# Kernel tuning notes

Hardware: AMD Instinct MI355X
Metric: run time of the kernel (lower is better)

Reference implementation:

```python
import jax, jax.numpy as jnp
import numpy as np

DN = ('NHWC', 'HWIO', 'NHWC')
EPS = 1e-3  # Keras BatchNormalization default epsilon


def conv2d(x, w):
    return jax.lax.conv_general_dilated(x, w, (1, 1), 'SAME', dimension_numbers=DN)


def hard_sigmoid(x):
    # Keras ConvLSTM2D default recurrent_activation
    return jnp.clip(0.2 * x + 0.5, 0.0, 1.0)


def convlstm2d(x, Wx, Wh, b):
    """Keras ConvLSTM2D, return_sequences=True. x: (B,T,H,W,C).
    Wx: (3,3,C,4F) input kernel, Wh: (3,3,F,4F) recurrent kernel, b: (4F,).
    Gate order (Keras): i, f, c, o."""
    B, T, H, W, C = x.shape
    F = Wh.shape[2]
    # input-to-gate convs for all timesteps in one batched conv
    xg = conv2d(x.reshape(B * T, H, W, C), Wx) + b          # (B*T,H,W,4F)
    xg = xg.reshape(B, T, H, W, 4 * F).transpose(1, 0, 2, 3, 4)  # (T,B,H,W,4F)

    def step(carry, xg_t):
        h, c = carry
        g = xg_t + conv2d(h, Wh)                            # (B,H,W,4F)
        i, f, cc, o = jnp.split(g, 4, axis=-1)
        i = hard_sigmoid(i)
        f = hard_sigmoid(f)
        o = hard_sigmoid(o)
        c = f * c + i * jnp.tanh(cc)
        h = o * jnp.tanh(c)
        return (h, c), h

    h0 = jnp.zeros((B, H, W, F), x.dtype)
    (_, _), hs = jax.lax.scan(step, (h0, h0), xg)           # hs: (T,B,H,W,F)
    return hs.transpose(1, 0, 2, 3, 4)


def batchnorm(x, gamma, beta):
    # training-mode BN over all axes except channel (last)
    mu = x.mean(axis=(0, 1, 2, 3), keepdims=True)
    var = x.var(axis=(0, 1, 2, 3), keepdims=True)
    return gamma * (x - mu) * jax.lax.rsqrt(var + EPS) + beta


def setup_inputs() -> dict:
    key = jax.random.key(0)
    B, T, H, W, C = 4, 8, 16, 16, 256
    F = 256
    ks = jax.random.split(key, 10)
    s = 0.02
    inp = {
        'input_tensor': jax.random.normal(ks[0], (B, T, H, W, C), jnp.float32),
        'Wx1': jax.random.normal(ks[1], (3, 3, C, 4 * F), jnp.float32) * s,
        'Wh1': jax.random.normal(ks[2], (3, 3, F, 4 * F), jnp.float32) * s,
        'b1': jnp.zeros((4 * F,), jnp.float32),
        'g1': jnp.ones((F,), jnp.float32),
        'be1': jnp.zeros((F,), jnp.float32),
        'Wx2': jax.random.normal(ks[3], (3, 3, F, 4 * F), jnp.float32) * s,
        'Wh2': jax.random.normal(ks[4], (3, 3, F, 4 * F), jnp.float32) * s,
        'b2': jnp.zeros((4 * F,), jnp.float32),
        'g2': jnp.ones((F,), jnp.float32),
        'be2': jnp.zeros((F,), jnp.float32),
        'Wx3': jax.random.normal(ks[5], (3, 3, F, 4 * F), jnp.float32) * s,
        'Wh3': jax.random.normal(ks[6], (3, 3, F, 4 * F), jnp.float32) * s,
        'b3': jnp.zeros((4 * F,), jnp.float32),
        'g3': jnp.ones((F,), jnp.float32),
        'be3': jnp.zeros((F,), jnp.float32),
    }
    return inp


def reference(input_tensor, Wx1, Wh1, b1, g1, be1,
              Wx2, Wh2, b2, g2, be2,
              Wx3, Wh3, b3, g3, be3):
    x = batchnorm(convlstm2d(input_tensor, Wx1, Wh1, b1), g1, be1)
    x = batchnorm(convlstm2d(x, Wx2, Wh2, b2), g2, be2)
    x = batchnorm(convlstm2d(x, Wx3, Wh3, b3), g3, be3)
    return x
```

## Files before the change

### kernel.cpp

```cpp
#include <hip/hip_runtime.h>

#define HW      256
#define COUT    1024
#define TSTEPS  8
#define BN_EPS  1e-3f
#define KTOT    2304

typedef unsigned short u16;
typedef unsigned int   u32;
typedef __attribute__((ext_vector_type(8))) _Float16 v8h;
typedef __attribute__((ext_vector_type(4))) float v4f;

__device__ __forceinline__ u16 f2h(float x) {
    _Float16 h = (_Float16)x; return *(u16*)&h;
}
__device__ __forceinline__ float h2f(u16 u) {
    _Float16 h = *(_Float16*)&u; return (float)h;
}
__device__ __forceinline__ float hsig(float x) {
    return fminf(fmaxf(0.2f * x + 0.5f, 0.f), 1.f);
}

typedef __attribute__((address_space(1))) const unsigned int gas_u32;
typedef __attribute__((address_space(3))) unsigned int las_u32;
__device__ __forceinline__ void gl16(const void* g, void* l) {
    __builtin_amdgcn_global_load_lds((gas_u32*)g, (las_u32*)l, 16, 0, 0);
}

__global__ __launch_bounds__(256, 2) void conv_big_k(
    const u16* __restrict__ apad,
    const u16* __restrict__ wT,
    const float* __restrict__ bias,
    u16* __restrict__ out)
{
    constexpr int KQ = 36;
    __shared__ u16 lds[2 * 16384];

    const int bid = blockIdx.x;
    const int xcd = bid & 7, idx = bid >> 3;
    const int by = (xcd >> 1) * 2 + (idx & 1);
    const int bx = (xcd & 1) * 32 + (idx >> 1);
    const int m0 = bx * 128, n0 = by * 128;
    const int tid = threadIdx.x, lane = tid & 63, w = tid >> 6;
    const int wr = w >> 1, wc = w & 1;
    const int lr = lane >> 3;
    const int g  = (lane & 7) ^ lr;
    const int fr = lane & 15, kc = lane >> 4;

    const char* a_src[4];
    #pragma unroll
    for (int i = 0; i < 4; ++i) {
        int m = m0 + w * 32 + i * 8 + lr;
        int img = m >> 8, pix = m & 255, yy = pix >> 4, xx = pix & 15;
        a_src[i] = (const char*)apad + ((((long)img * 18 + yy) * 18 + xx) * 256 + g * 8) * 2;
    }
    const char* b_src[4];
    #pragma unroll
    for (int i = 0; i < 4; ++i) {
        int n = n0 + w * 32 + i * 8 + lr;
        b_src[i] = (const char*)wT + ((long)n * KTOT + g * 8) * 2;
    }

    int aro[4][2], bro[4][2];
    #pragma unroll
    for (int mi = 0; mi < 4; ++mi) {
        int rl = wr * 64 + mi * 16 + fr;
        #pragma unroll
        for (int ks = 0; ks < 2; ++ks)
            aro[mi][ks] = rl * 128 + ((((ks << 2) | kc) ^ (fr & 7)) << 4);
    }
    #pragma unroll
    for (int ni = 0; ni < 4; ++ni) {
        int nr = wc * 64 + ni * 16 + fr;
        #pragma unroll
        for (int ks = 0; ks < 2; ++ks)
            bro[ni][ks] = 16384 + nr * 128 + ((((ks << 2) | kc) ^ (fr & 7)) << 4);
    }

    v4f acc[4][4];
    #pragma unroll
    for (int mi = 0; mi < 4; ++mi)
        #pragma unroll
        for (int ni = 0; ni < 4; ++ni) acc[mi][ni] = (v4f)0.f;

#define STAGE_B(J) { int j_ = (J); int dxy = j_ >> 2, c64 = j_ & 3;           \
    int dy = (dxy * 11) >> 5; int dx = dxy - dy * 3;                          \
    int aoff = ((dy * 18 + dx) * 256 + c64 * 64) * 2; int boff = j_ * 128;    \
    char* base = (char*)lds + (j_ & 1) * 32768;                               \
    _Pragma("unroll") for (int i = 0; i < 4; ++i)                             \
        gl16(a_src[i] + aoff, base + (w * 32 + i * 8) * 128);                 \
    _Pragma("unroll") for (int i = 0; i < 4; ++i)                             \
        gl16(b_src[i] + boff, base + 16384 + (w * 32 + i * 8) * 128); }

#define COMPUTE_B(J) { const char* base = (const char*)lds + ((J) & 1) * 32768; \
    v8h af[4][2], bf[4][2];                                                   \
    _Pragma("unroll") for (int mi = 0; mi < 4; ++mi)                          \
        _Pragma("unroll") for (int ks = 0; ks < 2; ++ks)                      \
            af[mi][ks] = *(const v8h*)(base + aro[mi][ks]);                   \
    _Pragma("unroll") for (int ni = 0; ni < 4; ++ni)                          \
        _Pragma("unroll") for (int ks = 0; ks < 2; ++ks)                      \
            bf[ni][ks] = *(const v8h*)(base + bro[ni][ks]);                   \
    __builtin_amdgcn_s_setprio(1);                                            \
    _Pragma("unroll") for (int ks = 0; ks < 2; ++ks)                          \
    _Pragma("unroll") for (int mi = 0; mi < 4; ++mi)                          \
    _Pragma("unroll") for (int ni = 0; ni < 4; ++ni)                          \
        acc[mi][ni] = __builtin_amdgcn_mfma_f32_16x16x32_f16(af[mi][ks], bf[ni][ks], acc[mi][ni], 0, 0, 0); \
    __builtin_amdgcn_s_setprio(0); }

    STAGE_B(0);
    for (int kq = 0; kq < KQ - 1; ++kq) {
        asm volatile("s_waitcnt vmcnt(0)" ::: "memory");
        __builtin_amdgcn_s_barrier();
        __builtin_amdgcn_sched_barrier(0);
        STAGE_B(kq + 1);
        COMPUTE_B(kq);
    }
    asm volatile("s_waitcnt vmcnt(0)" ::: "memory");
    __builtin_amdgcn_s_barrier();
    __builtin_amdgcn_sched_barrier(0);
    COMPUTE_B(KQ - 1);
#undef STAGE_B
#undef COMPUTE_B

    #pragma unroll
    for (int mi = 0; mi < 4; ++mi) {
        #pragma unroll
        for (int ni = 0; ni < 4; ++ni) {
            int mrow = m0 + wr * 64 + mi * 16 + ((lane >> 4) << 2);
            int ncol = n0 + wc * 64 + ni * 16 + fr;
            float b0 = bias[(ncol & 3) * 256 + (ncol >> 2)];
            #pragma unroll
            for (int r = 0; r < 4; ++r)
                out[(long)(mrow + r) * COUT + ncol] = f2h(acc[mi][ni][r] + b0);
        }
    }
}

__global__ __launch_bounds__(512) void rec_fused_k(
    const u16* __restrict__ ph_in,
    const u16* __restrict__ wTf,
    const u16* __restrict__ xg,
    float* __restrict__ cbuf,
    u16* __restrict__ hs16,
    u16* __restrict__ ph_out,
    int t)
{
    __shared__ u16 lds[6 * 4096];

    const int bid = blockIdx.x;
    const int by = (bid & 7) * 2 + ((bid >> 3) & 1);
    const int bx = bid >> 4;
    const int m0 = bx * 64, n0 = by * 64;
    const int tid = threadIdx.x, lane = tid & 63, w = tid >> 6;
    const int wr = w >> 2, wc = w & 3;
    const int fr = lane & 15, kc = lane >> 4;

    const int f4  = n0 + wc * 16 + (lane & 12);
    const int fch = f4 >> 2;
    int erow[2]; long xrow[2], cidx[2];
    uint2 xb_pre[2];
    float c_pre[2];
    #pragma unroll
    for (int mi = 0; mi < 2; ++mi) {
        erow[mi] = m0 + wr * 32 + mi * 16 + ((lane >> 4) << 2) + (lane & 3);
        int img = erow[mi] >> 8, pix = erow[mi] & 255;
        xrow[mi] = ((long)(img * TSTEPS + t) * HW + pix);
        cidx[mi] = (long)erow[mi] * 256 + fch;
        xb_pre[mi] = *(const uint2*)&xg[xrow[mi] * COUT + f4];
        c_pre[mi]  = cbuf[cidx[mi]];
    }

    const char* a_src;
    {
        int rt = tid >> 3;
        int gg = (tid & 7) ^ (rt & 7);
        int m = m0 + rt;
        int img = m >> 8, pix = m & 255, yy = pix >> 4, xx = pix & 15;
        a_src = (const char*)ph_in + ((((long)img * 18 + yy) * 18 + xx) * 256 + gg * 8) * 2;
    }
    const char* b_base = (const char*)wTf + ((long)(by * 4 + wc) * 72) * 1024 + lane * 16;

    int aro[2][2];
    #pragma unroll
    for (int mi = 0; mi < 2; ++mi)
        #pragma unroll
        for (int ks = 0; ks < 2; ++ks)
            aro[mi][ks] = (wr * 32 + mi * 16 + fr) * 128 + ((((ks << 2) | kc) ^ (fr & 7)) << 4);

    v4f acc0 = (v4f)0.f, acc1 = (v4f)0.f;

#define STAGE_A(J, BUF) { int j_ = (J); int dxy = j_ >> 2, c64 = j_ & 3;      \
    int dy = (dxy * 11) >> 5; int dx = dxy - dy * 3;                          \
    int aoff = ((dy * 18 + dx) * 256 + c64 * 64) * 2;                         \
    gl16(a_src + aoff, (char*)lds + (BUF) * 8192 + w * 1024); }

#define LDB(J, R0, R1) { R0 = *(const v8h*)(b_base + (2 * (J)) * 1024);       \
                         R1 = *(const v8h*)(b_base + (2 * (J) + 1) * 1024); }

#define CKQ(BUF, C0, C1) {                                                    \
    const char* base_ = (const char*)lds + (BUF) * 8192;                      \
    v8h af00_ = *(const v8h*)(base_ + aro[0][0]);                             \
    v8h af10_ = *(const v8h*)(base_ + aro[1][0]);                             \
    v8h af01_ = *(const v8h*)(base_ + aro[0][1]);                             \
    v8h af11_ = *(const v8h*)(base_ + aro[1][1]);                             \
    __builtin_amdgcn_s_setprio(1);                                            \
    acc0 = __builtin_amdgcn_mfma_f32_16x16x32_f16(af00_, C0, acc0, 0, 0, 0);  \
    acc1 = __builtin_amdgcn_mfma_f32_16x16x32_f16(af10_, C0, acc1, 0, 0, 0);  \
    acc0 = __builtin_amdgcn_mfma_f32_16x16x32_f16(af01_, C1, acc0, 0, 0, 0);  \
    acc1 = __builtin_amdgcn_mfma_f32_16x16x32_f16(af11_, C1, acc1, 0, 0, 0);  \
    __builtin_amdgcn_s_setprio(0); }

#define BODY2(J2, BC, BS, Ca0, Ca1, Cb0, Cb1, La0, La1, Lb0, Lb1) {           \
    int q0_ = 2 * (J2);                                                       \
    asm volatile("s_waitcnt vmcnt(6)" ::: "memory");                          \
    __builtin_amdgcn_s_barrier();                                             \
    __builtin_amdgcn_sched_barrier(0);                                        \
    LDB(q0_ + 4, La0, La1); LDB(q0_ + 5, Lb0, Lb1);                           \
    STAGE_A(q0_ + 4, BS); STAGE_A(q0_ + 5, (BS) + 1);                         \
    CKQ(BC,       Ca0, Ca1);                                                  \
    CKQ((BC) + 1, Cb0, Cb1); }

    v8h S00, S01, S02, S03, S10, S11, S12, S13, S20, S21, S22, S23;
    LDB(0, S00, S01); LDB(1, S02, S03); STAGE_A(0, 0); STAGE_A(1, 1);
    LDB(2, S10, S11); LDB(3, S12, S13); STAGE_A(2, 2); STAGE_A(3, 3);

    for (int j = 0; j < 5; ++j) {
        BODY2(3 * j,     0, 4, S00, S01, S02, S03, S20, S21, S22, S23);
        BODY2(3 * j + 1, 2, 0, S10, S11, S12, S13, S00, S01, S02, S03);
        BODY2(3 * j + 2, 4, 2, S20, S21, S22, S23, S10, S11, S12, S13);
    }
    BODY2(15, 0, 4, S00, S01, S02, S03, S20, S21, S22, S23);
    asm volatile("s_waitcnt vmcnt(6)" ::: "memory");
    __builtin_amdgcn_s_barrier();
    __builtin_amdgcn_sched_barrier(0);
    CKQ(2, S10, S11);
    CKQ(3, S12, S13);
    asm volatile("s_waitcnt vmcnt(0)" ::: "memory");
    __builtin_amdgcn_s_barrier();
    __builtin_amdgcn_sched_barrier(0);
    CKQ(4, S20, S21);
    CKQ(5, S22, S23);
#undef STAGE_A
#undef LDB
#undef CKQ
#undef BODY2

    v4f accA[2] = {acc0, acc1};
    const bool gl0 = lane & 1, gl1 = lane & 2;
    #pragma unroll
    for (int mi = 0; mi < 2; ++mi) {
        float V0 = accA[mi][0], V1 = accA[mi][1];
        float V2 = accA[mi][2], V3 = accA[mi][3];
        float x0 = __shfl_xor(V0, 1), x1 = __shfl_xor(V1, 1);
        float x2 = __shfl_xor(V2, 1), x3 = __shfl_xor(V3, 1);
        float a0 = gl0 ? x1 : V0;
        float a1 = gl0 ? V1 : x0;
        float a2 = gl0 ? x3 : V2;
        float a3 = gl0 ? V3 : x2;
        float s0 = __shfl_xor(a0, 2), s1 = __shfl_xor(a1, 2);
        float s2 = __shfl_xor(a2, 2), s3 = __shfl_xor(a3, 2);
        float Ti = gl1 ? s2 : a0;
        float Tf = gl1 ? s3 : a1;
        float Tc = gl1 ? a2 : s0;
        float To = gl1 ? a3 : s1;

        float pi = Ti + h2f((u16)(xb_pre[mi].x & 0xffff));
        float pf = Tf + h2f((u16)(xb_pre[mi].x >> 16));
        float pc = Tc + h2f((u16)(xb_pre[mi].y & 0xffff));
        float po = To + h2f((u16)(xb_pre[mi].y >> 16));
        float c = hsig(pf) * c_pre[mi] + hsig(pi) * tanhf(pc);
        float h = hsig(po) * tanhf(c);
        cbuf[cidx[mi]] = c;
        u16 hv = f2h(h);
        hs16[xrow[mi] * 256 + fch] = hv;
        int pix = erow[mi] & 255, img = erow[mi] >> 8;
        ph_out[(((long)img * 18 + (pix >> 4) + 1) * 18 + (pix & 15) + 1) * 256 + fch] = hv;
    }
}

__global__ __launch_bounds__(256) void gates0_k(
    const u16* __restrict__ xg, float* __restrict__ cbuf,
    u16* __restrict__ hs16, u16* __restrict__ ph_out)
{
    int idx = blockIdx.x * 256 + threadIdx.x;
    int fch = idx & 255, row = idx >> 8;
    int img = row >> 8, pix = row & 255;
    long xrow = (long)(img * TSTEPS) * HW + pix;
    uint2 xb = *(const uint2*)&xg[xrow * COUT + fch * 4];
    float pi = h2f((u16)(xb.x & 0xffff));
    float pc = h2f((u16)(xb.y & 0xffff));
    float po = h2f((u16)(xb.y >> 16));
    float c = hsig(pi) * tanhf(pc);
    float h = hsig(po) * tanhf(c);
    cbuf[(long)row * 256 + fch] = c;
    u16 hv = f2h(h);
    hs16[xrow * 256 + fch] = hv;
    int yy = pix >> 4, xx = pix & 15;
    ph_out[(((long)img * 18 + yy + 1) * 18 + xx + 1) * 256 + fch] = hv;
}

__global__ __launch_bounds__(256) void wprep_all_k(
    const float* __restrict__ wx, const float* __restrict__ wh,
    u16* __restrict__ wT, u16* __restrict__ wTf)
{
    int kq = blockIdx.x;
    int by = blockIdx.y;
    if (by < 4) {
        int k0 = kq * 32;
        int np = by * 256 + threadIdx.x;
        int n  = (np & 3) * 256 + (np >> 2);
        u32 pk[16];
        #pragma unroll
        for (int kk = 0; kk < 32; kk += 2) {
            float a = wx[(long)(k0 + kk) * COUT + n];
            float b = wx[(long)(k0 + kk + 1) * COUT + n];
            pk[kk >> 1] = (u32)f2h(a) | ((u32)f2h(b) << 16);
        }
        uint4* dst = (uint4*)&wT[(long)np * KTOT + k0];
        dst[0] = make_uint4(pk[0], pk[1], pk[2], pk[3]);
        dst[1] = make_uint4(pk[4], pk[5], pk[6], pk[7]);
        dst[2] = make_uint4(pk[8], pk[9], pk[10], pk[11]);
        dst[3] = make_uint4(pk[12], pk[13], pk[14], pk[15]);
    } else {
        int nf = (by - 4) * 4 + (threadIdx.x >> 6);
        int l  = threadIdx.x & 63;
        int np = nf * 16 + (l & 15);
        int n  = (np & 3) * 256 + (np >> 2);
        int k0 = kq * 32 + (l >> 4) * 8;
        u32 pk[4];
        #pragma unroll
        for (int e = 0; e < 8; e += 2) {
            float a = wh[(long)(k0 + e) * COUT + n];
            float b = wh[(long)(k0 + e + 1) * COUT + n];
            pk[e >> 1] = (u32)f2h(a) | ((u32)f2h(b) << 16);
        }
        *(uint4*)&wTf[((long)(nf * 72) + kq) * 512 + l * 8] =
            make_uint4(pk[0], pk[1], pk[2], pk[3]);
    }
}

__global__ __launch_bounds__(256) void convert_x_k(const float* __restrict__ x,
                                                   u16* __restrict__ padx)
{
    int q = blockIdx.x * 256 + threadIdx.x;
    int e0 = q * 4;
    int f = e0 & 255, pix = (e0 >> 8) & 255, img = e0 >> 16;
    float4 v = ((const float4*)x)[q];
    int yy = pix >> 4, xx = pix & 15;
    long o = (((long)img * 18 + yy + 1) * 18 + xx + 1) * 256 + f;
    u32 lo = (u32)f2h(v.x) | ((u32)f2h(v.y) << 16);
    u32 hi = (u32)f2h(v.z) | ((u32)f2h(v.w) << 16);
    *(uint2*)&padx[o] = make_uint2(lo, hi);
}

__global__ __launch_bounds__(256) void bn_stats1_k(
    const u16* __restrict__ x, float* __restrict__ partial)
{
    const int tid = threadIdx.x;
    const int blk = blockIdx.x;
    float s = 0.f, s2 = 0.f;
    const long base = (long)blk * 64 * 256;
    #pragma unroll 8
    for (int gi = 0; gi < 64; ++gi) {
        float v = h2f(x[base + gi * 256 + tid]);
        s += v; s2 += v * v;
    }
    partial[blk * 512 + tid]       = s;
    partial[blk * 512 + 256 + tid] = s2;
}

__global__ __launch_bounds__(256) void bn_stats2_k(
    const float* __restrict__ partial, const float* __restrict__ gamma,
    const float* __restrict__ beta, float* __restrict__ stats)
{
    const int f = threadIdx.x;
    float s = 0.f, s2 = 0.f;
    #pragma unroll 8
    for (int b = 0; b < 128; ++b) {
        s  += partial[b * 512 + f];
        s2 += partial[b * 512 + 256 + f];
    }
    const float inv_n = 1.f / 8192.f;
    float mu  = s * inv_n;
    float var = s2 * inv_n - mu * mu;
    float sc  = gamma[f] * rsqrtf(var + BN_EPS);
    stats[f]       = sc;
    stats[256 + f] = beta[f] - mu * sc;
}

__global__ __launch_bounds__(256) void bn_apply_k(
    const u16* __restrict__ x, const float* __restrict__ stats,
    u16* __restrict__ padx, float* __restrict__ out)
{
    const int q = blockIdx.x * 256 + threadIdx.x;
    const int e0 = q * 4;
    const int f = e0 & 255, pix = (e0 >> 8) & 255, img = e0 >> 16;
    ushort4 hv = ((const ushort4*)x)[q];
    float4 v = make_float4(h2f(hv.x), h2f(hv.y), h2f(hv.z), h2f(hv.w));
    float4 sc = *(const float4*)(stats + f);
    float4 sh = *(const float4*)(stats + 256 + f);
    v.x = v.x * sc.x + sh.x;
    v.y = v.y * sc.y + sh.y;
    v.z = v.z * sc.z + sh.z;
    v.w = v.w * sc.w + sh.w;
    if (out) ((float4*)out)[q] = v;
    if (padx) {
        int yy = pix >> 4, xx = pix & 15;
        long o = (((long)img * 18 + yy + 1) * 18 + xx + 1) * 256 + f;
        u32 lo = (u32)f2h(v.x) | ((u32)f2h(v.y) << 16);
        u32 hi = (u32)f2h(v.z) | ((u32)f2h(v.w) << 16);
        *(uint2*)&padx[o] = make_uint2(lo, hi);
    }
}

extern "C" void kernel_launch(void* const* d_in, const int* in_sizes, int n_in,
                              void* d_out, int out_size, void* d_ws, size_t ws_size,
                              hipStream_t stream)
{
    const float* x0    = (const float*)d_in[0];
    const float* Wx[3] = {(const float*)d_in[1], (const float*)d_in[6],  (const float*)d_in[11]};
    const float* Wh[3] = {(const float*)d_in[2], (const float*)d_in[7],  (const float*)d_in[12]};
    const float* bb[3] = {(const float*)d_in[3], (const float*)d_in[8],  (const float*)d_in[13]};
    const float* gg[3] = {(const float*)d_in[4], (const float*)d_in[9],  (const float*)d_in[14]};
    const float* be[3] = {(const float*)d_in[5], (const float*)d_in[10], (const float*)d_in[15]};

    float* ws    = (float*)d_ws;
    u16*  xg     = (u16*)ws;
    float* cbuf  = ws   + 4194304;
    u16*  hs16   = (u16*)(cbuf + 262144);
    float* part  = (float*)(hs16 + 2097152);
    float* stats = part + 65536;
    u16*  pad_x  = (u16*)(stats + 512);
    u16*  pad_h  = pad_x + 2654208;
    u16*  wTx    = pad_h + 663552;
    u16*  wTf    = wTx   + 2359296;
    const long PHN = 331776;

    hipMemsetAsync(pad_x, 0, 2654208 * sizeof(u16), stream);
    hipMemsetAsync(pad_h, 0, 2 * PHN * sizeof(u16), stream);
    hipLaunchKernelGGL(convert_x_k, dim3(2048), dim3(256), 0, stream, x0, pad_x);

    for (int l = 0; l < 3; ++l) {
        hipLaunchKernelGGL(wprep_all_k, dim3(72, 20), dim3(256), 0, stream,
            Wx[l], Wh[l], wTx, wTf);

        hipLaunchKernelGGL(conv_big_k, dim3(512), dim3(256), 0, stream,
            pad_x, wTx, bb[l], xg);

        hipLaunchKernelGGL(gates0_k, dim3(1024), dim3(256), 0, stream,
            xg, cbuf, hs16, pad_h + PHN);

        for (int t = 1; t < TSTEPS; ++t) {
            hipLaunchKernelGGL(rec_fused_k, dim3(256), dim3(512), 0, stream,
                pad_h + (t & 1) * PHN, wTf, xg, cbuf, hs16,
                pad_h + ((t & 1) ^ 1) * PHN, t);
        }

        hipLaunchKernelGGL(bn_stats1_k, dim3(128), dim3(256), 0, stream, hs16, part);
        hipLaunchKernelGGL(bn_stats2_k, dim3(1), dim3(256), 0, stream, part, gg[l], be[l], stats);
        hipLaunchKernelGGL(bn_apply_k, dim3(2048), dim3(256), 0, stream, hs16, stats,
            (l < 2) ? pad_x : (u16*)nullptr, (l == 2) ? (float*)d_out : (float*)nullptr);
    }
}
```

Measured before the change: 472.5 us.

## Retile recurrent conv kernel to 32x64 tiles with 256-thread blocks

The fused recurrent conv+LSTM kernel moves from 64x64 output tiles with 512 threads to 32x64 tiles with 256 threads, and launches 512 blocks instead of 256. Each wave now covers 16 rows by 32 columns, so it shares one A fragment across two B column chunks instead of one B chunk across two A row chunks. The goal is to fill more CUs for this small M=1024 GEMM and allow two blocks per CU. The cost is twice as many B weight loads per block in total and more register pressure from twelve extra prefetched B vectors.

```diff
diff --git a/kernel.cpp b/kernel.cpp
--- a/kernel.cpp
+++ b/kernel.cpp
@@ -136,7 +136,7 @@
     }
 }
 
-__global__ __launch_bounds__(512) void rec_fused_k(
+__global__ __launch_bounds__(256, 2) void rec_fused_k(
     const u16* __restrict__ ph_in,
     const u16* __restrict__ wTf,
     const u16* __restrict__ xg,
@@ -145,112 +145,120 @@
     u16* __restrict__ ph_out,
     int t)
 {
-    __shared__ u16 lds[6 * 4096];
+    __shared__ u16 lds[6 * 2048];
 
     const int bid = blockIdx.x;
     const int by = (bid & 7) * 2 + ((bid >> 3) & 1);
     const int bx = bid >> 4;
-    const int m0 = bx * 64, n0 = by * 64;
+    const int m0 = bx * 32, n0 = by * 64;
     const int tid = threadIdx.x, lane = tid & 63, w = tid >> 6;
-    const int wr = w >> 2, wc = w & 3;
+    const int wr = w >> 1, wc = w & 1;
     const int fr = lane & 15, kc = lane >> 4;
 
-    const int f4  = n0 + wc * 16 + (lane & 12);
-    const int fch = f4 >> 2;
-    int erow[2]; long xrow[2], cidx[2];
+    const int erow = m0 + wr * 16 + ((lane >> 4) << 2) + (lane & 3);
+    const int eimg = erow >> 8, epix = erow & 255;
+    const long xrow = ((long)(eimg * TSTEPS + t) * HW + epix);
+    int f4[2]; long cidx[2];
     uint2 xb_pre[2];
     float c_pre[2];
     #pragma unroll
-    for (int mi = 0; mi < 2; ++mi) {
-        erow[mi] = m0 + wr * 32 + mi * 16 + ((lane >> 4) << 2) + (lane & 3);
-        int img = erow[mi] >> 8, pix = erow[mi] & 255;
-        xrow[mi] = ((long)(img * TSTEPS + t) * HW + pix);
-        cidx[mi] = (long)erow[mi] * 256 + fch;
-        xb_pre[mi] = *(const uint2*)&xg[xrow[mi] * COUT + f4];
-        c_pre[mi]  = cbuf[cidx[mi]];
+    for (int ni = 0; ni < 2; ++ni) {
+        f4[ni] = n0 + wc * 32 + ni * 16 + (lane & 12);
+        cidx[ni] = (long)erow * 256 + (f4[ni] >> 2);
+        xb_pre[ni] = *(const uint2*)&xg[xrow * COUT + f4[ni]];
+        c_pre[ni]  = cbuf[cidx[ni]];
     }
 
     const char* a_src;
     {
-        int rt = tid >> 3;
-        int gg = (tid & 7) ^ (rt & 7);
+        int rt = w * 8 + (lane >> 3);
+        int gg = (lane & 7) ^ (lane >> 3);
         int m = m0 + rt;
         int img = m >> 8, pix = m & 255, yy = pix >> 4, xx = pix & 15;
         a_src = (const char*)ph_in + ((((long)img * 18 + yy) * 18 + xx) * 256 + gg * 8) * 2;
     }
-    const char* b_base = (const char*)wTf + ((long)(by * 4 + wc) * 72) * 1024 + lane * 16;
-
-    int aro[2][2];
-    #pragma unroll
-    for (int mi = 0; mi < 2; ++mi)
-        #pragma unroll
-        for (int ks = 0; ks < 2; ++ks)
-            aro[mi][ks] = (wr * 32 + mi * 16 + fr) * 128 + ((((ks << 2) | kc) ^ (fr & 7)) << 4);
+    const char* b_base0 = (const char*)wTf + ((long)(by * 4 + wc * 2 + 0) * 72) * 1024 + lane * 16;
+    const char* b_base1 = b_base0 + 72 * 1024;
+
+    int aro[2];
+    #pragma unroll
+    for (int ks = 0; ks < 2; ++ks)
+        aro[ks] = (wr * 16 + fr) * 128 + ((((ks << 2) | kc) ^ (fr & 7)) << 4);
 
     v4f acc0 = (v4f)0.f, acc1 = (v4f)0.f;
 
 #define STAGE_A(J, BUF) { int j_ = (J); int dxy = j_ >> 2, c64 = j_ & 3;      \
     int dy = (dxy * 11) >> 5; int dx = dxy - dy * 3;                          \
     int aoff = ((dy * 18 + dx) * 256 + c64 * 64) * 2;                         \
-    gl16(a_src + aoff, (char*)lds + (BUF) * 8192 + w * 1024); }
-
-#define LDB(J, R0, R1) { R0 = *(const v8h*)(b_base + (2 * (J)) * 1024);       \
-                         R1 = *(const v8h*)(b_base + (2 * (J) + 1) * 1024); }
-
-#define CKQ(BUF, C0, C1) {                                                    \
-    const char* base_ = (const char*)lds + (BUF) * 8192;                      \
-    v8h af00_ = *(const v8h*)(base_ + aro[0][0]);                             \
-    v8h af10_ = *(const v8h*)(base_ + aro[1][0]);                             \
-    v8h af01_ = *(const v8h*)(base_ + aro[0][1]);                             \
-    v8h af11_ = *(const v8h*)(base_ + aro[1][1]);                             \
+    gl16(a_src + aoff, (char*)lds + (BUF) * 4096 + w * 1024); }
+
+#define LDCH(J, R0, R1, R2, R3) {                                             \
+    R0 = *(const v8h*)(b_base0 + (2 * (J)) * 1024);                           \
+    R1 = *(const v8h*)(b_base0 + (2 * (J) + 1) * 1024);                       \
+    R2 = *(const v8h*)(b_base1 + (2 * (J)) * 1024);                           \
+    R3 = *(const v8h*)(b_base1 + (2 * (J) + 1) * 1024); }
+
+#define CKQ(BUF, R0, R1, R2, R3) {                                            \
+    const char* base_ = (const char*)lds + (BUF) * 4096;                      \
+    v8h af0_ = *(const v8h*)(base_ + aro[0]);                                 \
+    v8h af1_ = *(const v8h*)(base_ + aro[1]);                                 \
     __builtin_amdgcn_s_setprio(1);                                            \
-    acc0 = __builtin_amdgcn_mfma_f32_16x16x32_f16(af00_, C0, acc0, 0, 0, 0);  \
-    acc1 = __builtin_amdgcn_mfma_f32_16x16x32_f16(af10_, C0, acc1, 0, 0, 0);  \
-    acc0 = __builtin_amdgcn_mfma_f32_16x16x32_f16(af01_, C1, acc0, 0, 0, 0);  \
-    acc1 = __builtin_amdgcn_mfma_f32_16x16x32_f16(af11_, C1, acc1, 0, 0, 0);  \
+    acc0 = __builtin_amdgcn_mfma_f32_16x16x32_f16(af0_, R0, acc0, 0, 0, 0);   \
+    acc1 = __builtin_amdgcn_mfma_f32_16x16x32_f16(af0_, R2, acc1, 0, 0, 0);   \
+    acc0 = __builtin_amdgcn_mfma_f32_16x16x32_f16(af1_, R1, acc0, 0, 0, 0);   \
+    acc1 = __builtin_amdgcn_mfma_f32_16x16x32_f16(af1_, R3, acc1, 0, 0, 0);   \
     __builtin_amdgcn_s_setprio(0); }
 
-#define BODY2(J2, BC, BS, Ca0, Ca1, Cb0, Cb1, La0, La1, Lb0, Lb1) {           \
+#define BODY2(J2, BC, BS, A0,A1,A2,A3, B0,B1,B2,B3, LA0,LA1,LA2,LA3, LB0,LB1,LB2,LB3) { \
     int q0_ = 2 * (J2);                                                       \
-    asm volatile("s_waitcnt vmcnt(6)" ::: "memory");                          \
+    asm volatile("s_waitcnt vmcnt(10)" ::: "memory");                         \
     __builtin_amdgcn_s_barrier();                                             \
     __builtin_amdgcn_sched_barrier(0);                                        \
-    LDB(q0_ + 4, La0, La1); LDB(q0_ + 5, Lb0, Lb1);                           \
+    LDCH(q0_ + 4, LA0, LA1, LA2, LA3);                                        \
+    LDCH(q0_ + 5, LB0, LB1, LB2, LB3);                                        \
     STAGE_A(q0_ + 4, BS); STAGE_A(q0_ + 5, (BS) + 1);                         \
-    CKQ(BC,       Ca0, Ca1);                                                  \
-    CKQ((BC) + 1, Cb0, Cb1); }
-
-    v8h S00, S01, S02, S03, S10, S11, S12, S13, S20, S21, S22, S23;
-    LDB(0, S00, S01); LDB(1, S02, S03); STAGE_A(0, 0); STAGE_A(1, 1);
-    LDB(2, S10, S11); LDB(3, S12, S13); STAGE_A(2, 2); STAGE_A(3, 3);
+    CKQ(BC,       A0, A1, A2, A3);                                            \
+    CKQ((BC) + 1, B0, B1, B2, B3); }
+
+    v8h Pa0,Pa1,Pa2,Pa3, Pb0,Pb1,Pb2,Pb3;
+    v8h Qa0,Qa1,Qa2,Qa3, Qb0,Qb1,Qb2,Qb3;
+    v8h Ra0,Ra1,Ra2,Ra3, Rb0,Rb1,Rb2,Rb3;
+    LDCH(0, Pa0,Pa1,Pa2,Pa3); LDCH(1, Pb0,Pb1,Pb2,Pb3);
+    STAGE_A(0, 0); STAGE_A(1, 1);
+    LDCH(2, Qa0,Qa1,Qa2,Qa3); LDCH(3, Qb0,Qb1,Qb2,Qb3);
+    STAGE_A(2, 2); STAGE_A(3, 3);
 
     for (int j = 0; j < 5; ++j) {
-        BODY2(3 * j,     0, 4, S00, S01, S02, S03, S20, S21, S22, S23);
-        BODY2(3 * j + 1, 2, 0, S10, S11, S12, S13, S00, S01, S02, S03);
-        BODY2(3 * j + 2, 4, 2, S20, S21, S22, S23, S10, S11, S12, S13);
-    }
-    BODY2(15, 0, 4, S00, S01, S02, S03, S20, S21, S22, S23);
-    asm volatile("s_waitcnt vmcnt(6)" ::: "memory");
+        BODY2(3 * j,     0, 4, Pa0,Pa1,Pa2,Pa3, Pb0,Pb1,Pb2,Pb3,
+                               Ra0,Ra1,Ra2,Ra3, Rb0,Rb1,Rb2,Rb3);
+        BODY2(3 * j + 1, 2, 0, Qa0,Qa1,Qa2,Qa3, Qb0,Qb1,Qb2,Qb3,
+                               Pa0,Pa1,Pa2,Pa3, Pb0,Pb1,Pb2,Pb3);
+        BODY2(3 * j + 2, 4, 2, Ra0,Ra1,Ra2,Ra3, Rb0,Rb1,Rb2,Rb3,
+                               Qa0,Qa1,Qa2,Qa3, Qb0,Qb1,Qb2,Qb3);
+    }
+    BODY2(15, 0, 4, Pa0,Pa1,Pa2,Pa3, Pb0,Pb1,Pb2,Pb3,
+                    Ra0,Ra1,Ra2,Ra3, Rb0,Rb1,Rb2,Rb3);
+    asm volatile("s_waitcnt vmcnt(10)" ::: "memory");
     __builtin_amdgcn_s_barrier();
     __builtin_amdgcn_sched_barrier(0);
-    CKQ(2, S10, S11);
-    CKQ(3, S12, S13);
+    CKQ(2, Qa0,Qa1,Qa2,Qa3);
+    CKQ(3, Qb0,Qb1,Qb2,Qb3);
     asm volatile("s_waitcnt vmcnt(0)" ::: "memory");
     __builtin_amdgcn_s_barrier();
     __builtin_amdgcn_sched_barrier(0);
-    CKQ(4, S20, S21);
-    CKQ(5, S22, S23);
+    CKQ(4, Ra0,Ra1,Ra2,Ra3);
+    CKQ(5, Rb0,Rb1,Rb2,Rb3);
 #undef STAGE_A
-#undef LDB
+#undef LDCH
 #undef CKQ
 #undef BODY2
 
     v4f accA[2] = {acc0, acc1};
     const bool gl0 = lane & 1, gl1 = lane & 2;
     #pragma unroll
-    for (int mi = 0; mi < 2; ++mi) {
-        float V0 = accA[mi][0], V1 = accA[mi][1];
-        float V2 = accA[mi][2], V3 = accA[mi][3];
+    for (int ni = 0; ni < 2; ++ni) {
+        float V0 = accA[ni][0], V1 = accA[ni][1];
+        float V2 = accA[ni][2], V3 = accA[ni][3];
         float x0 = __shfl_xor(V0, 1), x1 = __shfl_xor(V1, 1);
         float x2 = __shfl_xor(V2, 1), x3 = __shfl_xor(V3, 1);
         float a0 = gl0 ? x1 : V0;
@@ -264,17 +272,17 @@
         float Tc = gl1 ? a2 : s0;
         float To = gl1 ? a3 : s1;
 
-        float pi = Ti + h2f((u16)(xb_pre[mi].x & 0xffff));
-        float pf = Tf + h2f((u16)(xb_pre[mi].x >> 16));
-        float pc = Tc + h2f((u16)(xb_pre[mi].y & 0xffff));
-        float po = To + h2f((u16)(xb_pre[mi].y >> 16));
-        float c = hsig(pf) * c_pre[mi] + hsig(pi) * tanhf(pc);
+        float pi = Ti + h2f((u16)(xb_pre[ni].x & 0xffff));
+        float pf = Tf + h2f((u16)(xb_pre[ni].x >> 16));
+        float pc = Tc + h2f((u16)(xb_pre[ni].y & 0xffff));
+        float po = To + h2f((u16)(xb_pre[ni].y >> 16));
+        float c = hsig(pf) * c_pre[ni] + hsig(pi) * tanhf(pc);
         float h = hsig(po) * tanhf(c);
-        cbuf[cidx[mi]] = c;
+        cbuf[cidx[ni]] = c;
         u16 hv = f2h(h);
-        hs16[xrow[mi] * 256 + fch] = hv;
-        int pix = erow[mi] & 255, img = erow[mi] >> 8;
-        ph_out[(((long)img * 18 + (pix >> 4) + 1) * 18 + (pix & 15) + 1) * 256 + fch] = hv;
+        int fch = f4[ni] >> 2;
+        hs16[xrow * 256 + fch] = hv;
+        ph_out[(((long)eimg * 18 + (epix >> 4) + 1) * 18 + (epix & 15) + 1) * 256 + fch] = hv;
     }
 }
 
@@ -451,7 +459,7 @@
             xg, cbuf, hs16, pad_h + PHN);
 
         for (int t = 1; t < TSTEPS; ++t) {
-            hipLaunchKernelGGL(rec_fused_k, dim3(256), dim3(512), 0, stream,
+            hipLaunchKernelGGL(rec_fused_k, dim3(512), dim3(256), 0, stream,
                 pad_h + (t & 1) * PHN, wTf, xg, cbuf, hs16,
                 pad_h + ((t & 1) ^ 1) * PHN, t);
         }
```

After: 529.1 us. +12.0%, slower.

## Load conv weights directly to registers in fragment layout with deeper A pipeline

Applied to the files above, without the earlier changes.

The input-to-gate conv kernel now loads B (weights) straight from global memory into registers, using the MFMA fragment-major layout that the recurrent kernel already used. Only A tiles are staged in LDS, through a 6-buffer pipeline that keeps several chunks in flight (vmcnt(12)). The block grows to 512 threads with 8 waves in a 2x4 grid, each wave owning 4x2 MFMA tiles, and the XCD-aware block swizzle is dropped. The aim is to cut LDS traffic and barrier stalls. The cost is more register pressure, one block per CU, and global weight reads repeated across waves.

```diff
diff --git a/kernel.cpp b/kernel.cpp
--- a/kernel.cpp
+++ b/kernel.cpp
@@ -27,107 +27,141 @@
     __builtin_amdgcn_global_load_lds((gas_u32*)g, (las_u32*)l, 16, 0, 0);
 }
 
-__global__ __launch_bounds__(256, 2) void conv_big_k(
+__global__ __launch_bounds__(512, 1) void conv_big_k(
     const u16* __restrict__ apad,
-    const u16* __restrict__ wT,
+    const u16* __restrict__ wTxf,
     const float* __restrict__ bias,
     u16* __restrict__ out)
 {
-    constexpr int KQ = 36;
-    __shared__ u16 lds[2 * 16384];
+    __shared__ u16 lds[6 * 8192];
 
     const int bid = blockIdx.x;
-    const int xcd = bid & 7, idx = bid >> 3;
-    const int by = (xcd >> 1) * 2 + (idx & 1);
-    const int bx = (xcd & 1) * 32 + (idx >> 1);
+    const int by = bid & 7, bx = bid >> 3;
     const int m0 = bx * 128, n0 = by * 128;
     const int tid = threadIdx.x, lane = tid & 63, w = tid >> 6;
-    const int wr = w >> 1, wc = w & 1;
-    const int lr = lane >> 3;
-    const int g  = (lane & 7) ^ lr;
+    const int wr = w >> 2, wc = w & 3;
     const int fr = lane & 15, kc = lane >> 4;
 
-    const char* a_src[4];
-    #pragma unroll
-    for (int i = 0; i < 4; ++i) {
-        int m = m0 + w * 32 + i * 8 + lr;
+    const char *a_src0, *a_src1;
+    {
+        int gg = (lane & 7) ^ (lane >> 3);
+        int rt = w * 16 + (lane >> 3);
+        int m = m0 + rt;
         int img = m >> 8, pix = m & 255, yy = pix >> 4, xx = pix & 15;
-        a_src[i] = (const char*)apad + ((((long)img * 18 + yy) * 18 + xx) * 256 + g * 8) * 2;
-    }
-    const char* b_src[4];
-    #pragma unroll
-    for (int i = 0; i < 4; ++i) {
-        int n = n0 + w * 32 + i * 8 + lr;
-        b_src[i] = (const char*)wT + ((long)n * KTOT + g * 8) * 2;
-    }
-
-    int aro[4][2], bro[4][2];
-    #pragma unroll
-    for (int mi = 0; mi < 4; ++mi) {
-        int rl = wr * 64 + mi * 16 + fr;
+        a_src0 = (const char*)apad + ((((long)img * 18 + yy) * 18 + xx) * 256 + gg * 8) * 2;
+        m += 8; img = m >> 8; pix = m & 255; yy = pix >> 4; xx = pix & 15;
+        a_src1 = (const char*)apad + ((((long)img * 18 + yy) * 18 + xx) * 256 + gg * 8) * 2;
+    }
+    const char* bb0 = (const char*)wTxf + ((long)(by * 8 + wc * 2) * 72) * 1024 + lane * 16;
+    const char* bb1 = bb0 + 72 * 1024;
+
+    int aro[4][2];
+    #pragma unroll
+    for (int mi = 0; mi < 4; ++mi)
         #pragma unroll
         for (int ks = 0; ks < 2; ++ks)
-            aro[mi][ks] = rl * 128 + ((((ks << 2) | kc) ^ (fr & 7)) << 4);
-    }
-    #pragma unroll
-    for (int ni = 0; ni < 4; ++ni) {
-        int nr = wc * 64 + ni * 16 + fr;
-        #pragma unroll
-        for (int ks = 0; ks < 2; ++ks)
-            bro[ni][ks] = 16384 + nr * 128 + ((((ks << 2) | kc) ^ (fr & 7)) << 4);
-    }
-
-    v4f acc[4][4];
-    #pragma unroll
-    for (int mi = 0; mi < 4; ++mi)
-        #pragma unroll
-        for (int ni = 0; ni < 4; ++ni) acc[mi][ni] = (v4f)0.f;
-
-#define STAGE_B(J) { int j_ = (J); int dxy = j_ >> 2, c64 = j_ & 3;           \
+            aro[mi][ks] = (wr * 64 + mi * 16 + fr) * 128 + ((((ks << 2) | kc) ^ (fr & 7)) << 4);
+
+    v4f acc[4][2];
+    #pragma unroll
+    for (int mi = 0; mi < 4; ++mi) {
+        acc[mi][0] = (v4f)0.f;
+        acc[mi][1] = (v4f)0.f;
+    }
+
+#define STAGE_C(C, BUF) { int c_ = (C); int dxy = c_ >> 2, c64 = c_ & 3;      \
     int dy = (dxy * 11) >> 5; int dx = dxy - dy * 3;                          \
-    int aoff = ((dy * 18 + dx) * 256 + c64 * 64) * 2; int boff = j_ * 128;    \
-    char* base = (char*)lds + (j_ & 1) * 32768;                               \
-    _Pragma("unroll") for (int i = 0; i < 4; ++i)                             \
-        gl16(a_src[i] + aoff, base + (w * 32 + i * 8) * 128);                 \
-    _Pragma("unroll") for (int i = 0; i < 4; ++i)                             \
-        gl16(b_src[i] + boff, base + 16384 + (w * 32 + i * 8) * 128); }
-
-#define COMPUTE_B(J) { const char* base = (const char*)lds + ((J) & 1) * 32768; \
-    v8h af[4][2], bf[4][2];                                                   \
-    _Pragma("unroll") for (int mi = 0; mi < 4; ++mi)                          \
-        _Pragma("unroll") for (int ks = 0; ks < 2; ++ks)                      \
-            af[mi][ks] = *(const v8h*)(base + aro[mi][ks]);                   \
-    _Pragma("unroll") for (int ni = 0; ni < 4; ++ni)                          \
-        _Pragma("unroll") for (int ks = 0; ks < 2; ++ks)                      \
-            bf[ni][ks] = *(const v8h*)(base + bro[ni][ks]);                   \
+    int aoff = ((dy * 18 + dx) * 256 + c64 * 64) * 2;                         \
+    char* dst = (char*)lds + (BUF) * 16384 + w * 2048;                        \
+    gl16(a_src0 + aoff, dst); gl16(a_src1 + aoff, dst + 1024); }
+
+#define LDCH(C, R0, R1, R2, R3) { int kq_ = 2 * (C);                          \
+    R0 = *(const v8h*)(bb0 + (long)kq_ * 1024);                               \
+    R1 = *(const v8h*)(bb1 + (long)kq_ * 1024);                               \
+    R2 = *(const v8h*)(bb0 + (long)(kq_ + 1) * 1024);                         \
+    R3 = *(const v8h*)(bb1 + (long)(kq_ + 1) * 1024); }
+
+#define CCH(BUF, R0, R1, R2, R3) {                                            \
+    const char* base_ = (const char*)lds + (BUF) * 16384;                     \
+    v8h a00_ = *(const v8h*)(base_ + aro[0][0]);                              \
+    v8h a10_ = *(const v8h*)(base_ + aro[1][0]);                              \
+    v8h a20_ = *(const v8h*)(base_ + aro[2][0]);                              \
+    v8h a30_ = *(const v8h*)(base_ + aro[3][0]);                              \
     __builtin_amdgcn_s_setprio(1);                                            \
-    _Pragma("unroll") for (int ks = 0; ks < 2; ++ks)                          \
-    _Pragma("unroll") for (int mi = 0; mi < 4; ++mi)                          \
-    _Pragma("unroll") for (int ni = 0; ni < 4; ++ni)                          \
-        acc[mi][ni] = __builtin_amdgcn_mfma_f32_16x16x32_f16(af[mi][ks], bf[ni][ks], acc[mi][ni], 0, 0, 0); \
+    acc[0][0] = __builtin_amdgcn_mfma_f32_16x16x32_f16(a00_, R0, acc[0][0], 0, 0, 0); \
+    acc[0][1] = __builtin_amdgcn_mfma_f32_16x16x32_f16(a00_, R1, acc[0][1], 0, 0, 0); \
+    acc[1][0] = __builtin_amdgcn_mfma_f32_16x16x32_f16(a10_, R0, acc[1][0], 0, 0, 0); \
+    acc[1][1] = __builtin_amdgcn_mfma_f32_16x16x32_f16(a10_, R1, acc[1][1], 0, 0, 0); \
+    acc[2][0] = __builtin_amdgcn_mfma_f32_16x16x32_f16(a20_, R0, acc[2][0], 0, 0, 0); \
+    acc[2][1] = __builtin_amdgcn_mfma_f32_16x16x32_f16(a20_, R1, acc[2][1], 0, 0, 0); \
+    acc[3][0] = __builtin_amdgcn_mfma_f32_16x16x32_f16(a30_, R0, acc[3][0], 0, 0, 0); \
+    acc[3][1] = __builtin_amdgcn_mfma_f32_16x16x32_f16(a30_, R1, acc[3][1], 0, 0, 0); \
+    __builtin_amdgcn_s_setprio(0);                                            \
+    v8h a01_ = *(const v8h*)(base_ + aro[0][1]);                              \
+    v8h a11_ = *(const v8h*)(base_ + aro[1][1]);                              \
+    v8h a21_ = *(const v8h*)(base_ + aro[2][1]);                              \
+    v8h a31_ = *(const v8h*)(base_ + aro[3][1]);                              \
+    __builtin_amdgcn_s_setprio(1);                                            \
+    acc[0][0] = __builtin_amdgcn_mfma_f32_16x16x32_f16(a01_, R2, acc[0][0], 0, 0, 0); \
+    acc[0][1] = __builtin_amdgcn_mfma_f32_16x16x32_f16(a01_, R3, acc[0][1], 0, 0, 0); \
+    acc[1][0] = __builtin_amdgcn_mfma_f32_16x16x32_f16(a11_, R2, acc[1][0], 0, 0, 0); \
+    acc[1][1] = __builtin_amdgcn_mfma_f32_16x16x32_f16(a11_, R3, acc[1][1], 0, 0, 0); \
+    acc[2][0] = __builtin_amdgcn_mfma_f32_16x16x32_f16(a21_, R2, acc[2][0], 0, 0, 0); \
+    acc[2][1] = __builtin_amdgcn_mfma_f32_16x16x32_f16(a21_, R3, acc[2][1], 0, 0, 0); \
+    acc[3][0] = __builtin_amdgcn_mfma_f32_16x16x32_f16(a31_, R2, acc[3][0], 0, 0, 0); \
+    acc[3][1] = __builtin_amdgcn_mfma_f32_16x16x32_f16(a31_, R3, acc[3][1], 0, 0, 0); \
     __builtin_amdgcn_s_setprio(0); }
 
-    STAGE_B(0);
-    for (int kq = 0; kq < KQ - 1; ++kq) {
-        asm volatile("s_waitcnt vmcnt(0)" ::: "memory");
-        __builtin_amdgcn_s_barrier();
-        __builtin_amdgcn_sched_barrier(0);
-        STAGE_B(kq + 1);
-        COMPUTE_B(kq);
-    }
+#define BODY_C(J, BC, BS, A0,A1,A2,A3, B0,B1,B2,B3, LA0,LA1,LA2,LA3, LB0,LB1,LB2,LB3) { \
+    int c0_ = 2 * (J);                                                        \
+    asm volatile("s_waitcnt vmcnt(12)" ::: "memory");                         \
+    __builtin_amdgcn_s_barrier();                                             \
+    __builtin_amdgcn_sched_barrier(0);                                        \
+    LDCH(c0_ + 4, LA0, LA1, LA2, LA3);                                        \
+    LDCH(c0_ + 5, LB0, LB1, LB2, LB3);                                        \
+    STAGE_C(c0_ + 4, BS); STAGE_C(c0_ + 5, (BS) + 1);                         \
+    CCH(BC,       A0, A1, A2, A3);                                            \
+    CCH((BC) + 1, B0, B1, B2, B3); }
+
+    v8h Pa0,Pa1,Pa2,Pa3, Pb0,Pb1,Pb2,Pb3;
+    v8h Qa0,Qa1,Qa2,Qa3, Qb0,Qb1,Qb2,Qb3;
+    v8h Ra0,Ra1,Ra2,Ra3, Rb0,Rb1,Rb2,Rb3;
+    LDCH(0, Pa0,Pa1,Pa2,Pa3); LDCH(1, Pb0,Pb1,Pb2,Pb3);
+    STAGE_C(0, 0); STAGE_C(1, 1);
+    LDCH(2, Qa0,Qa1,Qa2,Qa3); LDCH(3, Qb0,Qb1,Qb2,Qb3);
+    STAGE_C(2, 2); STAGE_C(3, 3);
+
+    for (int j = 0; j < 5; ++j) {
+        BODY_C(3 * j,     0, 4, Pa0,Pa1,Pa2,Pa3, Pb0,Pb1,Pb2,Pb3,
+                                Ra0,Ra1,Ra2,Ra3, Rb0,Rb1,Rb2,Rb3);
+        BODY_C(3 * j + 1, 2, 0, Qa0,Qa1,Qa2,Qa3, Qb0,Qb1,Qb2,Qb3,
+                                Pa0,Pa1,Pa2,Pa3, Pb0,Pb1,Pb2,Pb3);
+        BODY_C(3 * j + 2, 4, 2, Ra0,Ra1,Ra2,Ra3, Rb0,Rb1,Rb2,Rb3,
+                                Qa0,Qa1,Qa2,Qa3, Qb0,Qb1,Qb2,Qb3);
+    }
+    BODY_C(15, 0, 4, Pa0,Pa1,Pa2,Pa3, Pb0,Pb1,Pb2,Pb3,
+                     Ra0,Ra1,Ra2,Ra3, Rb0,Rb1,Rb2,Rb3);
+    asm volatile("s_waitcnt vmcnt(12)" ::: "memory");
+    __builtin_amdgcn_s_barrier();
+    __builtin_amdgcn_sched_barrier(0);
+    CCH(2, Qa0,Qa1,Qa2,Qa3);
+    CCH(3, Qb0,Qb1,Qb2,Qb3);
     asm volatile("s_waitcnt vmcnt(0)" ::: "memory");
     __builtin_amdgcn_s_barrier();
     __builtin_amdgcn_sched_barrier(0);
-    COMPUTE_B(KQ - 1);
-#undef STAGE_B
-#undef COMPUTE_B
+    CCH(4, Ra0,Ra1,Ra2,Ra3);
+    CCH(5, Rb0,Rb1,Rb2,Rb3);
+#undef STAGE_C
+#undef LDCH
+#undef CCH
+#undef BODY_C
 
     #pragma unroll
     for (int mi = 0; mi < 4; ++mi) {
         #pragma unroll
-        for (int ni = 0; ni < 4; ++ni) {
+        for (int ni = 0; ni < 2; ++ni) {
             int mrow = m0 + wr * 64 + mi * 16 + ((lane >> 4) << 2);
-            int ncol = n0 + wc * 64 + ni * 16 + fr;
+            int ncol = n0 + wc * 32 + ni * 16 + fr;
             float b0 = bias[(ncol & 3) * 256 + (ncol >> 2)];
             #pragma unroll
             for (int r = 0; r < 4; ++r)
@@ -301,42 +335,26 @@
 
 __global__ __launch_bounds__(256) void wprep_all_k(
     const float* __restrict__ wx, const float* __restrict__ wh,
-    u16* __restrict__ wT, u16* __restrict__ wTf)
+    u16* __restrict__ wTxf, u16* __restrict__ wTf)
 {
     int kq = blockIdx.x;
     int by = blockIdx.y;
-    if (by < 4) {
-        int k0 = kq * 32;
-        int np = by * 256 + threadIdx.x;
-        int n  = (np & 3) * 256 + (np >> 2);
-        u32 pk[16];
-        #pragma unroll
-        for (int kk = 0; kk < 32; kk += 2) {
-            float a = wx[(long)(k0 + kk) * COUT + n];
-            float b = wx[(long)(k0 + kk + 1) * COUT + n];
-            pk[kk >> 1] = (u32)f2h(a) | ((u32)f2h(b) << 16);
-        }
-        uint4* dst = (uint4*)&wT[(long)np * KTOT + k0];
-        dst[0] = make_uint4(pk[0], pk[1], pk[2], pk[3]);
-        dst[1] = make_uint4(pk[4], pk[5], pk[6], pk[7]);
-        dst[2] = make_uint4(pk[8], pk[9], pk[10], pk[11]);
-        dst[3] = make_uint4(pk[12], pk[13], pk[14], pk[15]);
-    } else {
-        int nf = (by - 4) * 4 + (threadIdx.x >> 6);
-        int l  = threadIdx.x & 63;
-        int np = nf * 16 + (l & 15);
-        int n  = (np & 3) * 256 + (np >> 2);
-        int k0 = kq * 32 + (l >> 4) * 8;
-        u32 pk[4];
-        #pragma unroll
-        for (int e = 0; e < 8; e += 2) {
-            float a = wh[(long)(k0 + e) * COUT + n];
-            float b = wh[(long)(k0 + e + 1) * COUT + n];
-            pk[e >> 1] = (u32)f2h(a) | ((u32)f2h(b) << 16);
-        }
-        *(uint4*)&wTf[((long)(nf * 72) + kq) * 512 + l * 8] =
-            make_uint4(pk[0], pk[1], pk[2], pk[3]);
-    }
+    const float* src = (by < 16) ? wx : wh;
+    u16* dst = (by < 16) ? wTxf : wTf;
+    int nf = ((by & 15) * 4) + (threadIdx.x >> 6);
+    int l  = threadIdx.x & 63;
+    int np = nf * 16 + (l & 15);
+    int n  = (np & 3) * 256 + (np >> 2);
+    int k0 = kq * 32 + (l >> 4) * 8;
+    u32 pk[4];
+    #pragma unroll
+    for (int e = 0; e < 8; e += 2) {
+        float a = src[(long)(k0 + e) * COUT + n];
+        float b = src[(long)(k0 + e + 1) * COUT + n];
+        pk[e >> 1] = (u32)f2h(a) | ((u32)f2h(b) << 16);
+    }
+    *(uint4*)&dst[((long)(nf * 72) + kq) * 512 + l * 8] =
+        make_uint4(pk[0], pk[1], pk[2], pk[3]);
 }
 
 __global__ __launch_bounds__(256) void convert_x_k(const float* __restrict__ x,
@@ -432,8 +450,8 @@
     float* stats = part + 65536;
     u16*  pad_x  = (u16*)(stats + 512);
     u16*  pad_h  = pad_x + 2654208;
-    u16*  wTx    = pad_h + 663552;
-    u16*  wTf    = wTx   + 2359296;
+    u16*  wTxf   = pad_h + 663552;
+    u16*  wTf    = wTxf  + 2359296;
     const long PHN = 331776;
 
     hipMemsetAsync(pad_x, 0, 2654208 * sizeof(u16), stream);
@@ -441,11 +459,11 @@
     hipLaunchKernelGGL(convert_x_k, dim3(2048), dim3(256), 0, stream, x0, pad_x);
 
     for (int l = 0; l < 3; ++l) {
-        hipLaunchKernelGGL(wprep_all_k, dim3(72, 20), dim3(256), 0, stream,
-            Wx[l], Wh[l], wTx, wTf);
-
-        hipLaunchKernelGGL(conv_big_k, dim3(512), dim3(256), 0, stream,
-            pad_x, wTx, bb[l], xg);
+        hipLaunchKernelGGL(wprep_all_k, dim3(72, 32), dim3(256), 0, stream,
+            Wx[l], Wh[l], wTxf, wTf);
+
+        hipLaunchKernelGGL(conv_big_k, dim3(512), dim3(512), 0, stream,
+            pad_x, wTxf, bb[l], xg);
 
         hipLaunchKernelGGL(gates0_k, dim3(1024), dim3(256), 0, stream,
             xg, cbuf, hs16, pad_h + PHN);
```

Measured after the change: 519.0 us. 1.1x slower.
